# Performance work log

Measured on AMD Instinct MI355X. Metric: run time of the kernel, lower is better.

## Reference

```python
import jax, jax.numpy as jnp
import numpy as np

B, L, D, DF, E, R = 4, 1024, 1024, 4096, 32768, 64
EPS = 1e-6


def layer_norm(x, g, b, eps=EPS):
    mu = x.mean(-1, keepdims=True)
    var = ((x - mu) ** 2).mean(-1, keepdims=True)
    return (x - mu) * jax.lax.rsqrt(var + eps) * g + b


def setup_inputs() -> dict:
    key = jax.random.key(0)
    ks = jax.random.split(key, 16)
    s = 0.02
    return {
        "hidden_states": jax.random.normal(ks[0], (B, L, D), jnp.float32),
        "rel_table": jax.random.normal(ks[1], (R, D), jnp.float32) * s,
        "Wq": jax.random.normal(ks[2], (D, D), jnp.float32) * s,
        "bq": jnp.zeros((D,), jnp.float32),
        "Wk": jax.random.normal(ks[3], (D, D), jnp.float32) * s,
        "Wv": jax.random.normal(ks[4], (D, D), jnp.float32) * s,
        "Wo": jax.random.normal(ks[5], (D, D), jnp.float32) * s,
        "bo": jnp.zeros((D,), jnp.float32),
        "ln0_g": jnp.ones((D,), jnp.float32),
        "ln0_b": jnp.zeros((D,), jnp.float32),
        "ln1_g": jnp.ones((D,), jnp.float32),
        "ln1_b": jnp.zeros((D,), jnp.float32),
        "W1": jax.random.normal(ks[6], (D, DF), jnp.float32) * s,
        "b1": jnp.zeros((DF,), jnp.float32),
        "W2": jax.random.normal(ks[7], (DF, D), jnp.float32) * s,
        "b2": jnp.zeros((D,), jnp.float32),
        "ln2_g": jnp.ones((D,), jnp.float32),
        "ln2_b": jnp.zeros((D,), jnp.float32),
        "edge_src": jax.random.randint(ks[8], (B, E), 0, L, jnp.int32),
        "edge_dst": jax.random.randint(ks[9], (B, E), 0, L, jnp.int32),
        "edge_rel": jax.random.randint(ks[10], (B, E), 0, R, jnp.int32),
    }


def reference(hidden_states, rel_table, Wq, bq, Wk, Wv, Wo, bo,
              ln0_g, ln0_b, ln1_g, ln1_b, W1, b1, W2, b2, ln2_g, ln2_b,
              edge_src, edge_dst, edge_rel):
    scale = np.sqrt(D).astype(np.float32)  # num_heads=1 -> d_k = D
    hs_norm = layer_norm(hidden_states, ln0_g, ln0_b)

    def rgat_one(x, src, dst, rel):
        # x: [L, D]; src/dst/rel: [E]
        e = rel_table[rel]                       # [E, D] relation embeddings
        q = x @ Wq + bq
        k = x @ Wk
        v = x @ Wv
        score = jnp.sum((k[src] + e) * q[dst], axis=-1) / scale      # [E]
        score = jnp.exp(jnp.clip(score, -10.0, 10.0))
        wv = jax.ops.segment_sum((v[src] + e) * score[:, None], dst, num_segments=L)
        z = jax.ops.segment_sum(score, dst, num_segments=L)          # [L]
        o = wv / z[:, None]
        out = layer_norm(x + o @ Wo + bo, ln1_g, ln1_b)
        ffn = jnp.maximum(out @ W1 + b1, 0.0) @ W2 + b2
        return layer_norm(out + ffn, ln2_g, ln2_b)

    graph_rep = jax.vmap(rgat_one)(hs_norm, edge_src, edge_dst, edge_rel)
    out = jax.nn.elu(graph_rep)                  # dropout = identity (eval)
    return hidden_states + out
```

## Files before the change

### kernel.cpp

```cpp
#include <hip/hip_runtime.h>
#include <hip/hip_bf16.h>

#define B_SZ 4
#define L_SEQ 1024
#define D_MODEL 1024
#define DF_FF 4096
#define E_PER_B 32768
#define R_REL 64
#define M_ROWS (B_SZ * L_SEQ)

typedef __attribute__((ext_vector_type(8))) short bf16x8;
typedef __attribute__((ext_vector_type(4))) float f32x4;

__device__ inline float b2f(unsigned short u) {
    union { unsigned int i; float f; } x; x.i = ((unsigned int)u) << 16; return x.f;
}
__device__ inline unsigned short f2b(float f) {
    union { float f; unsigned int u; } x; x.f = f;
    unsigned int r = x.u + 0x7FFFu + ((x.u >> 16) & 1u);
    return (unsigned short)(r >> 16);
}

#define GLOBAL_CAST(p) ((const __attribute__((address_space(1))) void*)(p))
#define LDS_CAST(p)    ((__attribute__((address_space(3))) void*)(p))

__global__ void prep_all(const float* __restrict__ Wq, const float* __restrict__ Wk,
                         const float* __restrict__ Wv, const float* __restrict__ Wo,
                         const float* __restrict__ W1, const float* __restrict__ W2,
                         const float* __restrict__ rel, const float* __restrict__ bq,
                         unsigned short* __restrict__ Wqkv_t, unsigned short* __restrict__ Wo_t,
                         unsigned short* __restrict__ W1_t, unsigned short* __restrict__ W2_t,
                         unsigned short* __restrict__ relbPad, unsigned short* __restrict__ relbT,
                         float* __restrict__ bqkv) {
    __shared__ float tile[32][33];
    const int id = blockIdx.x, tid = threadIdx.x;
    if (id < 12288) {
        const float* src; unsigned short* dst; int K, N, x, y;
        if (id < 4096) {
            const int seg = id >> 10, t = id & 1023;
            K = 1024; N = 1024; x = t & 31; y = t >> 5;
            src = (seg == 0) ? Wq : (seg == 1) ? Wk : (seg == 2) ? Wv : Wo;
            dst = (seg == 3) ? Wo_t : (Wqkv_t + (size_t)seg * 1048576);
        } else if (id < 8192) {
            const int t = id - 4096; K = 1024; N = 4096; x = t & 127; y = t >> 7;
            src = W1; dst = W1_t;
        } else {
            const int t = id - 8192; K = 4096; N = 1024; x = t & 31; y = t >> 5;
            src = W2; dst = W2_t;
        }
        const int n0 = x * 32, k0 = y * 32, tx = tid & 31, ty = tid >> 5;
#pragma unroll
        for (int r = 0; r < 32; r += 8)
            tile[ty + r][tx] = src[(size_t)(k0 + ty + r) * N + (n0 + tx)];
        __syncthreads();
#pragma unroll
        for (int r = 0; r < 32; r += 8)
            dst[(size_t)(n0 + ty + r) * K + (k0 + tx)] = f2b(tile[tx][ty + r]);
    } else if (id < 12800) {
        const int i = (id - 12288) * 256 + tid;
        relbPad[i] = (i < 65536) ? f2b(rel[i]) : (unsigned short)0;
    } else if (id < 13056) {
        const int i = (id - 12800) * 256 + tid;
        relbT[i] = f2b(rel[(i & 63) * 1024 + (i >> 6)]);
    } else {
        const int i = (id - 13056) * 256 + tid;
        bqkv[i] = (i < 1024) ? bq[i] : 0.0f;
    }
}

__global__ void transpose_v_bf16(const unsigned short* __restrict__ QKV,
                                 unsigned short* __restrict__ Vt) {
    __shared__ unsigned short tile[32][33];
    const int b = blockIdx.z;
    const int d0 = blockIdx.x * 32, s0 = blockIdx.y * 32;
    const int tx = threadIdx.x & 31, ty = threadIdx.x >> 5;
#pragma unroll
    for (int r = 0; r < 32; r += 8)
        tile[ty + r][tx] = QKV[(size_t)((b << 10) + s0 + ty + r) * 3072 + 2048 + d0 + tx];
    __syncthreads();
#pragma unroll
    for (int r = 0; r < 32; r += 8)
        Vt[(size_t)b * 1048576 + (size_t)(d0 + ty + r) * 1024 + s0 + tx] = tile[tx][ty + r];
}

__device__ inline void tile_swizzle(int id, int ntn, int& tm, int& tn) {
    tm = ((id & 7) + ((id >> 3) / ntn) * 8) * 128;
    tn = ((id >> 3) % ntn) * 128;
}

template<bool OUT_BF16, bool RELU, bool ACC>
__global__ __launch_bounds__(256, 4)
void gemm_bf16(const unsigned short* __restrict__ A, int lda,
               const unsigned short* __restrict__ Bt, int ldb, size_t bt_batch,
               const float* __restrict__ bias,
               float* __restrict__ Cf, unsigned short* __restrict__ Cb,
               const float* __restrict__ accin,
               int N, int K, int ntn) {
    __shared__ unsigned short lA[128 * 64];
    __shared__ unsigned short lB[128 * 64];
    int tile_m, tile_n;
    tile_swizzle(blockIdx.x, ntn, tile_m, tile_n);
    const int t = threadIdx.x;
    const int wave = t >> 6, lane = t & 63;
    const int wm = (wave >> 1) * 64, wn = (wave & 1) * 64;
    const int quad = lane >> 4, l16 = lane & 15;

    const int srow = lane >> 3;
    const int schunk = ((lane & 7) ^ srow) * 8;
    const unsigned short* gA = A + (size_t)(tile_m + wave * 32 + srow) * lda + schunk;
    const unsigned short* gB = Bt + (size_t)(tile_m >> 10) * bt_batch
                                  + (size_t)(tile_n + wave * 32 + srow) * ldb + schunk;

    f32x4 acc[4][4];
#pragma unroll
    for (int i = 0; i < 4; i++)
#pragma unroll
        for (int j = 0; j < 4; j++) acc[i][j] = (f32x4)0.0f;

    for (int k0 = 0; k0 < K; k0 += 64) {
        __syncthreads();
#pragma unroll
        for (int r = 0; r < 4; ++r) {
            __builtin_amdgcn_global_load_lds(GLOBAL_CAST(gA + (size_t)r * 8 * lda),
                                             LDS_CAST(&lA[(wave * 32 + r * 8) * 64]), 16, 0, 0);
            __builtin_amdgcn_global_load_lds(GLOBAL_CAST(gB + (size_t)r * 8 * ldb),
                                             LDS_CAST(&lB[(wave * 32 + r * 8) * 64]), 16, 0, 0);
        }
        gA += 64; gB += 64;
        __builtin_amdgcn_s_waitcnt(0);
        __syncthreads();

#pragma unroll
        for (int kk = 0; kk < 2; ++kk) {
            const int cb = kk * 4 + quad;
            bf16x8 af[4], bf[4];
#pragma unroll
            for (int i = 0; i < 4; i++) {
                const int ra = wm + i * 16 + l16;
                af[i] = *(const bf16x8*)&lA[ra * 64 + ((cb ^ (ra & 7)) * 8)];
                const int rb = wn + i * 16 + l16;
                bf[i] = *(const bf16x8*)&lB[rb * 64 + ((cb ^ (rb & 7)) * 8)];
            }
#pragma unroll
            for (int mi = 0; mi < 4; mi++)
#pragma unroll
                for (int ni = 0; ni < 4; ni++)
                    acc[mi][ni] = __builtin_amdgcn_mfma_f32_16x16x32_bf16(af[mi], bf[ni], acc[mi][ni], 0, 0, 0);
        }
    }

#pragma unroll
    for (int mi = 0; mi < 4; mi++) {
#pragma unroll
        for (int ni = 0; ni < 4; ni++) {
            const int col = tile_n + wn + ni * 16 + l16;
            const float bv = bias[col];
#pragma unroll
            for (int r = 0; r < 4; r++) {
                const int row = tile_m + wm + mi * 16 + quad * 4 + r;
                float v = acc[mi][ni][r] + bv;
                if (ACC) v += accin[(size_t)row * N + col];
                if (RELU) v = fmaxf(v, 0.0f);
                if (OUT_BF16) Cb[(size_t)row * N + col] = f2b(v);
                else          Cf[(size_t)row * N + col] = v;
            }
        }
    }
}

__global__ __launch_bounds__(256, 4)
void gemm_bf16_splitk(const unsigned short* __restrict__ A, int lda,
                      const unsigned short* __restrict__ Bt, int ldb, size_t bt_batch,
                      const float* __restrict__ bias,
                      unsigned short* __restrict__ Pbase, size_t pstride,
                      int N, int Kc, int ntn) {
    __shared__ unsigned short lA[128 * 64];
    __shared__ unsigned short lB[128 * 64];
    int tile_m, tile_n;
    tile_swizzle(blockIdx.x, ntn, tile_m, tile_n);
    const int z = blockIdx.z;
    const int kofs = z * Kc;
    const int t = threadIdx.x;
    const int wave = t >> 6, lane = t & 63;
    const int wm = (wave >> 1) * 64, wn = (wave & 1) * 64;
    const int quad = lane >> 4, l16 = lane & 15;

    const int srow = lane >> 3;
    const int schunk = ((lane & 7) ^ srow) * 8;
    const unsigned short* gA = A + (size_t)(tile_m + wave * 32 + srow) * lda + kofs + schunk;
    const unsigned short* gB = Bt + (size_t)(tile_m >> 10) * bt_batch
                                  + (size_t)(tile_n + wave * 32 + srow) * ldb + kofs + schunk;

    f32x4 acc[4][4];
#pragma unroll
    for (int i = 0; i < 4; i++)
#pragma unroll
        for (int j = 0; j < 4; j++) acc[i][j] = (f32x4)0.0f;

    for (int k0 = 0; k0 < Kc; k0 += 64) {
        __syncthreads();
#pragma unroll
        for (int r = 0; r < 4; ++r) {
            __builtin_amdgcn_global_load_lds(GLOBAL_CAST(gA + (size_t)r * 8 * lda),
                                             LDS_CAST(&lA[(wave * 32 + r * 8) * 64]), 16, 0, 0);
            __builtin_amdgcn_global_load_lds(GLOBAL_CAST(gB + (size_t)r * 8 * ldb),
                                             LDS_CAST(&lB[(wave * 32 + r * 8) * 64]), 16, 0, 0);
        }
        gA += 64; gB += 64;
        __builtin_amdgcn_s_waitcnt(0);
        __syncthreads();

#pragma unroll
        for (int kk = 0; kk < 2; ++kk) {
            const int cb = kk * 4 + quad;
            bf16x8 af[4], bf[4];
#pragma unroll
            for (int i = 0; i < 4; i++) {
                const int ra = wm + i * 16 + l16;
                af[i] = *(const bf16x8*)&lA[ra * 64 + ((cb ^ (ra & 7)) * 8)];
                const int rb = wn + i * 16 + l16;
                bf[i] = *(const bf16x8*)&lB[rb * 64 + ((cb ^ (rb & 7)) * 8)];
            }
#pragma unroll
            for (int mi = 0; mi < 4; mi++)
#pragma unroll
                for (int ni = 0; ni < 4; ni++)
                    acc[mi][ni] = __builtin_amdgcn_mfma_f32_16x16x32_bf16(af[mi], bf[ni], acc[mi][ni], 0, 0, 0);
        }
    }

    unsigned short* P = Pbase + (size_t)z * pstride;
#pragma unroll
    for (int mi = 0; mi < 4; mi++) {
#pragma unroll
        for (int ni = 0; ni < 4; ni++) {
            const int col = tile_n + wn + ni * 16 + l16;
            const float bv = (z == 0) ? bias[col] : 0.0f;
#pragma unroll
            for (int r = 0; r < 4; r++) {
                const int row = tile_m + wm + mi * 16 + quad * 4 + r;
                P[(size_t)row * N + col] = f2b(acc[mi][ni][r] + bv);
            }
        }
    }
}

template<int MODE, int NR>
__global__ void ln_kernel(const float* __restrict__ X, const unsigned short* __restrict__ Xb,
                          const unsigned short* __restrict__ Rbase, size_t rstride,
                          const float* __restrict__ g, const float* __restrict__ be,
                          float* __restrict__ of32, unsigned short* __restrict__ ob16,
                          const float* __restrict__ hidden, float* __restrict__ fout) {
    __shared__ float sb1[4], sb2[4];
    const int row = blockIdx.x, t = threadIdx.x;
    const size_t base = (size_t)row * 1024 + t * 4;

    float x0, x1, x2, x3;
    if (MODE == 2) {
        ushort4 xv = *(const ushort4*)(Xb + base);
        x0 = b2f(xv.x); x1 = b2f(xv.y); x2 = b2f(xv.z); x3 = b2f(xv.w);
    } else {
        float4 xv = *(const float4*)(X + base);
        x0 = xv.x; x1 = xv.y; x2 = xv.z; x3 = xv.w;
    }
#pragma unroll
    for (int r = 0; r < NR; r++) {
        ushort4 rv = *(const ushort4*)(Rbase + r * rstride + base);
        x0 += b2f(rv.x); x1 += b2f(rv.y); x2 += b2f(rv.z); x3 += b2f(rv.w);
    }
    float s = x0 + x1 + x2 + x3;
#pragma unroll
    for (int o = 32; o > 0; o >>= 1) s += __shfl_down(s, o);
    if ((t & 63) == 0) sb1[t >> 6] = s;
    __syncthreads();
    const float mu = (sb1[0] + sb1[1] + sb1[2] + sb1[3]) * (1.0f / 1024.0f);

    const float d0 = x0 - mu, d1 = x1 - mu, d2 = x2 - mu, d3 = x3 - mu;
    float s2 = d0 * d0 + d1 * d1 + d2 * d2 + d3 * d3;
#pragma unroll
    for (int o = 32; o > 0; o >>= 1) s2 += __shfl_down(s2, o);
    if ((t & 63) == 0) sb2[t >> 6] = s2;
    __syncthreads();
    const float var = (sb2[0] + sb2[1] + sb2[2] + sb2[3]) * (1.0f / 1024.0f);
    const float rstd = rsqrtf(var + 1e-6f);

    const float4 gv = *(const float4*)(g + t * 4);
    const float4 bv = *(const float4*)(be + t * 4);
    const float y0 = d0 * rstd * gv.x + bv.x;
    const float y1 = d1 * rstd * gv.y + bv.y;
    const float y2 = d2 * rstd * gv.z + bv.z;
    const float y3 = d3 * rstd * gv.w + bv.w;

    if (MODE == 0) {
        float4 o; o.x = y0; o.y = y1; o.z = y2; o.w = y3;
        *(float4*)(of32 + base) = o;
    }
    if (MODE <= 1) {
        ushort4 ob; ob.x = f2b(y0); ob.y = f2b(y1); ob.z = f2b(y2); ob.w = f2b(y3);
        *(ushort4*)(ob16 + base) = ob;
    } else {
        const float4 hv = *(const float4*)(hidden + base);
        const float e0 = y0 > 0.0f ? y0 : expm1f(y0);
        const float e1 = y1 > 0.0f ? y1 : expm1f(y1);
        const float e2 = y2 > 0.0f ? y2 : expm1f(y2);
        const float e3 = y3 > 0.0f ? y3 : expm1f(y3);
        float4 o; o.x = hv.x + e0; o.y = hv.y + e1; o.z = hv.z + e2; o.w = hv.w + e3;
        *(float4*)(fout + base) = o;
    }
}

__global__ void edge_scatter(const unsigned short* __restrict__ S0h,
                             const unsigned short* __restrict__ S1h,
                             const float* __restrict__ T,
                             const int* __restrict__ src, const int* __restrict__ dst,
                             const int* __restrict__ rel,
                             float* __restrict__ A, float* __restrict__ G) {
    const int gg = blockIdx.x * 256 + threadIdx.x;
    const int b = gg >> 15;
    const int s = src[gg], d = dst[gg], r = rel[gg];
    const size_t srow = (size_t)((b << 10) + s) * 1024 + d;
    const float sval = b2f(S0h[srow]) + b2f(S1h[srow]);
    const float tval = T[(size_t)((b << 10) + d) * 128 + r];
    float sc = (sval + tval) * (1.0f / 32.0f);
    sc = expf(fminf(fmaxf(sc, -10.0f), 10.0f));
    atomicAdd(&A[((size_t)((b << 10) + d) << 10) + s], sc);
    atomicAdd(&G[((size_t)((b << 10) + d) << 6) + r], sc);
}

__global__ void normalize(const float* __restrict__ A, const float* __restrict__ G,
                          unsigned short* __restrict__ An, unsigned short* __restrict__ Gn) {
    __shared__ float sInv;
    const int row = blockIdx.x, t = threadIdx.x;
    float v = 0.0f;
    if (t < 64) {
        v = G[(size_t)row * 64 + t];
        float s = v;
#pragma unroll
        for (int o = 1; o < 64; o <<= 1) s += __shfl_xor(s, o);
        if (t == 0) sInv = 1.0f / s;
    }
    __syncthreads();
    const float inv = sInv;
    if (t < 64) Gn[(size_t)row * 64 + t] = f2b(v * inv);
    const size_t base = (size_t)row * 1024 + t * 4;
    const float4 a = *(const float4*)(A + base);
    ushort4 o;
    o.x = f2b(a.x * inv); o.y = f2b(a.y * inv); o.z = f2b(a.z * inv); o.w = f2b(a.w * inv);
    *(ushort4*)(An + base) = o;
}

extern "C" void kernel_launch(void* const* d_in, const int* in_sizes, int n_in,
                              void* d_out, int out_size, void* d_ws, size_t ws_size,
                              hipStream_t stream) {
    const float* hidden  = (const float*)d_in[0];
    const float* rel_tbl = (const float*)d_in[1];
    const float* Wq = (const float*)d_in[2];
    const float* bq = (const float*)d_in[3];
    const float* Wk = (const float*)d_in[4];
    const float* Wv = (const float*)d_in[5];
    const float* Wo = (const float*)d_in[6];
    const float* bo = (const float*)d_in[7];
    const float* ln0_g = (const float*)d_in[8];
    const float* ln0_b = (const float*)d_in[9];
    const float* ln1_g = (const float*)d_in[10];
    const float* ln1_b = (const float*)d_in[11];
    const float* W1 = (const float*)d_in[12];
    const float* b1 = (const float*)d_in[13];
    const float* W2 = (const float*)d_in[14];
    const float* b2 = (const float*)d_in[15];
    const float* ln2_g = (const float*)d_in[16];
    const float* ln2_b = (const float*)d_in[17];
    const int* esrc = (const int*)d_in[18];
    const int* edst = (const int*)d_in[19];
    const int* erel = (const int*)d_in[20];
    float* out = (float*)d_out;

    char* ws = (char*)d_ws;
    const size_t MB = 1024 * 1024;
    float*          Xn_f32  = (float*)(ws + 0);
    unsigned short* Xn_b16  = (unsigned short*)(ws + 16 * MB);
    unsigned short* Vt      = (unsigned short*)(ws + 16 * MB);
    unsigned short* H1      = (unsigned short*)(ws + 0);
    unsigned short* Wqkv_t  = (unsigned short*)(ws + 24 * MB);
    unsigned short* Wo_t    = (unsigned short*)(ws + 30 * MB);
    unsigned short* W1_t    = (unsigned short*)(ws + 32 * MB);
    unsigned short* W2_t    = (unsigned short*)(ws + 40 * MB);
    unsigned short* relbPad = (unsigned short*)(ws + 48 * MB);
    unsigned short* relbT   = (unsigned short*)(ws + 48 * MB + 256 * 1024);
    float*          bqkv    = (float*)(ws + 48 * MB + 512 * 1024);
    const float*    zbias   = bqkv + 1024;
    unsigned short* QKV     = (unsigned short*)(ws + 49 * MB);
    float*          Amat    = (float*)(ws + 49 * MB);
    float*          Gmat    = (float*)(ws + 65 * MB);
    unsigned short* PwoH    = (unsigned short*)(ws + 49 * MB);
    unsigned short* Qw2H    = (unsigned short*)(ws + 49 * MB);
    unsigned short* S0h     = (unsigned short*)(ws + 73 * MB);
    float*          tmp     = (float*)(ws + 73 * MB);
    unsigned short* Obf     = (unsigned short*)(ws + 89 * MB);
    unsigned short* An      = (unsigned short*)(ws + 97 * MB);
    float*          Tmat    = (float*)(ws + 105 * MB);
    unsigned short* Gn      = (unsigned short*)(ws + 105 * MB);
    unsigned short* Out_b16 = (unsigned short*)(ws + 113 * MB);

    const size_t PSTRIDE_H = 4u * 1024 * 1024;
    const size_t BT_QKV  = 1024u * 3072;
    const size_t BT_VT   = 1024u * 1024;
    const dim3 blk(256);

    prep_all<<<13068, blk, 0, stream>>>(Wq, Wk, Wv, Wo, W1, W2, rel_tbl, bq,
                                        Wqkv_t, Wo_t, W1_t, W2_t, relbPad, relbT, bqkv);
    ln_kernel<0, 0><<<M_ROWS, blk, 0, stream>>>(hidden, nullptr, nullptr, 0, ln0_g, ln0_b,
                                                Xn_f32, Xn_b16, nullptr, nullptr);
    gemm_bf16<true, false, false><<<dim3(24 * 32), blk, 0, stream>>>(
        Xn_b16, 1024, Wqkv_t, 1024, 0, bqkv, nullptr, QKV, nullptr, 3072, 1024, 24);
    transpose_v_bf16<<<dim3(32, 32, 4), blk, 0, stream>>>(QKV, Vt);
    gemm_bf16_splitk<<<dim3(8 * 32, 1, 2), blk, 0, stream>>>(
        QKV + 1024, 3072, QKV, 3072, BT_QKV, zbias, S0h, PSTRIDE_H, 1024, 512, 8);
    gemm_bf16<false, false, false><<<dim3(1 * 32), blk, 0, stream>>>(
        QKV, 3072, relbPad, 1024, 0, zbias, Tmat, nullptr, nullptr, 128, 1024, 1);
    hipMemsetAsync(ws + 49 * MB, 0, 17 * MB, stream);
    edge_scatter<<<512, blk, 0, stream>>>(S0h, S0h + PSTRIDE_H, Tmat, esrc, edst, erel, Amat, Gmat);
    normalize<<<M_ROWS, blk, 0, stream>>>(Amat, Gmat, An, Gn);
    gemm_bf16<false, false, false><<<dim3(8 * 32), blk, 0, stream>>>(
        Gn, 64, relbT, 64, 0, zbias, tmp, nullptr, nullptr, 1024, 64, 8);
    gemm_bf16<true, false, true><<<dim3(8 * 32), blk, 0, stream>>>(
        An, 1024, Vt, 1024, BT_VT, zbias, nullptr, Obf, tmp, 1024, 1024, 8);
    gemm_bf16_splitk<<<dim3(8 * 32, 1, 2), blk, 0, stream>>>(
        Obf, 1024, Wo_t, 1024, 0, bo, PwoH, PSTRIDE_H, 1024, 512, 8);
    ln_kernel<1, 2><<<M_ROWS, blk, 0, stream>>>(Xn_f32, nullptr, PwoH, PSTRIDE_H, ln1_g, ln1_b,
                                                nullptr, Out_b16, nullptr, nullptr);
    gemm_bf16<true, true, false><<<dim3(32 * 32), blk, 0, stream>>>(
        Out_b16, 1024, W1_t, 1024, 0, b1, nullptr, H1, nullptr, 4096, 1024, 32);
    gemm_bf16_splitk<<<dim3(8 * 32, 1, 4), blk, 0, stream>>>(
        H1, 4096, W2_t, 4096, 0, b2, Qw2H, PSTRIDE_H, 1024, 1024, 8);
    ln_kernel<2, 4><<<M_ROWS, blk, 0, stream>>>(nullptr, Out_b16, Qw2H, PSTRIDE_H, ln2_g, ln2_b,
                                                nullptr, nullptr, hidden, out);
    (void)in_sizes; (void)n_in; (void)out_size; (void)ws_size;
}
```

Before: 402.0 us.

## Fuse relation-term GEMMs into extended score and aggregation GEMMs

The K·Q score GEMM and the Q·rel table GEMM are merged into one extended GEMM (1152 rows per batch) whose output layout lets the edge scatter read both terms from one buffer. The aggregation now concatenates the attention matrix with the normalized relation weights along K (1088 wide) and the transposed V with the transposed relation table, so a single GEMM replaces the small G·rel GEMM plus the accumulate-in pass. This removes two launches and an fp32 intermediate round trip. In exchange the relation term is now stored in bf16 instead of fp32, and K=1088 is not a multiple of 128, which relies on the GEMM handling a 64-step K.

```diff
diff --git a/kernel.cpp b/kernel.cpp
--- a/kernel.cpp
+++ b/kernel.cpp
@@ -24,13 +24,18 @@
 #define GLOBAL_CAST(p) ((const __attribute__((address_space(1))) void*)(p))
 #define LDS_CAST(p)    ((__attribute__((address_space(3))) void*)(p))
 
+#define LDB_WV 1088
+#define BT_WV  (1024u * 1088u)
+#define BT_QKV (1024u * 3072u)
+#define SEXT_M 1152
+
 __global__ void prep_all(const float* __restrict__ Wq, const float* __restrict__ Wk,
                          const float* __restrict__ Wv, const float* __restrict__ Wo,
                          const float* __restrict__ W1, const float* __restrict__ W2,
                          const float* __restrict__ rel, const float* __restrict__ bq,
                          unsigned short* __restrict__ Wqkv_t, unsigned short* __restrict__ Wo_t,
                          unsigned short* __restrict__ W1_t, unsigned short* __restrict__ W2_t,
-                         unsigned short* __restrict__ relbPad, unsigned short* __restrict__ relbT,
+                         unsigned short* __restrict__ relbPad, unsigned short* __restrict__ Bwv,
                          float* __restrict__ bqkv) {
     __shared__ float tile[32][33];
     const int id = blockIdx.x, tid = threadIdx.x;
@@ -59,17 +64,18 @@
     } else if (id < 12800) {
         const int i = (id - 12288) * 256 + tid;
         relbPad[i] = (i < 65536) ? f2b(rel[i]) : (unsigned short)0;
-    } else if (id < 13056) {
+    } else if (id < 13824) {
         const int i = (id - 12800) * 256 + tid;
-        relbT[i] = f2b(rel[(i & 63) * 1024 + (i >> 6)]);
+        const int b = i >> 16, rem = i & 65535, d = rem >> 6, r = rem & 63;
+        Bwv[(size_t)b * BT_WV + (size_t)d * LDB_WV + 1024 + r] = f2b(rel[r * 1024 + d]);
     } else {
-        const int i = (id - 13056) * 256 + tid;
+        const int i = (id - 13824) * 256 + tid;
         bqkv[i] = (i < 1024) ? bq[i] : 0.0f;
     }
 }
 
 __global__ void transpose_v_bf16(const unsigned short* __restrict__ QKV,
-                                 unsigned short* __restrict__ Vt) {
+                                 unsigned short* __restrict__ Bwv) {
     __shared__ unsigned short tile[32][33];
     const int b = blockIdx.z;
     const int d0 = blockIdx.x * 32, s0 = blockIdx.y * 32;
@@ -80,7 +86,7 @@
     __syncthreads();
 #pragma unroll
     for (int r = 0; r < 32; r += 8)
-        Vt[(size_t)b * 1048576 + (size_t)(d0 + ty + r) * 1024 + s0 + tx] = tile[tx][ty + r];
+        Bwv[(size_t)b * BT_WV + (size_t)(d0 + ty + r) * LDB_WV + s0 + tx] = tile[tx][ty + r];
 }
 
 __device__ inline void tile_swizzle(int id, int ntn, int& tm, int& tn) {
@@ -88,13 +94,12 @@
     tn = ((id >> 3) % ntn) * 128;
 }
 
-template<bool OUT_BF16, bool RELU, bool ACC>
+template<bool OUT_BF16, bool RELU>
 __global__ __launch_bounds__(256, 4)
 void gemm_bf16(const unsigned short* __restrict__ A, int lda,
                const unsigned short* __restrict__ Bt, int ldb, size_t bt_batch,
                const float* __restrict__ bias,
                float* __restrict__ Cf, unsigned short* __restrict__ Cb,
-               const float* __restrict__ accin,
                int N, int K, int ntn) {
     __shared__ unsigned short lA[128 * 64];
     __shared__ unsigned short lB[128 * 64];
@@ -159,7 +164,6 @@
             for (int r = 0; r < 4; r++) {
                 const int row = tile_m + wm + mi * 16 + quad * 4 + r;
                 float v = acc[mi][ni][r] + bv;
-                if (ACC) v += accin[(size_t)row * N + col];
                 if (RELU) v = fmaxf(v, 0.0f);
                 if (OUT_BF16) Cb[(size_t)row * N + col] = f2b(v);
                 else          Cf[(size_t)row * N + col] = v;
@@ -245,6 +249,89 @@
     }
 }
 
+__global__ __launch_bounds__(256, 4)
+void gemm_sext(const unsigned short* __restrict__ QKV,
+               const unsigned short* __restrict__ relPad,
+               unsigned short* __restrict__ Pbase, int Kc) {
+    __shared__ unsigned short lA[128 * 64];
+    __shared__ unsigned short lB[128 * 64];
+    const int bx = blockIdx.x, b = blockIdx.y, z = blockIdx.z;
+    const int tile_m = (bx >> 3) * 128;
+    const int tile_n = (bx & 7) * 128;
+    const int kofs = z * Kc;
+    const int t = threadIdx.x;
+    const int wave = t >> 6, lane = t & 63;
+    const int wm = (wave >> 1) * 64, wn = (wave & 1) * 64;
+    const int quad = lane >> 4, l16 = lane & 15;
+
+    const int srow = lane >> 3;
+    const int schunk = ((lane & 7) ^ srow) * 8;
+    const int arow = tile_m + wave * 32 + srow;
+    const unsigned short* gA;
+    size_t lda;
+    if (tile_m < 1024) {
+        gA = QKV + (size_t)b * BT_QKV + (size_t)arow * 3072 + 1024 + kofs + schunk;
+        lda = 3072;
+    } else {
+        gA = relPad + (size_t)(arow - 1024) * 1024 + kofs + schunk;
+        lda = 1024;
+    }
+    const unsigned short* gB = QKV + (size_t)b * BT_QKV
+                                   + (size_t)(tile_n + wave * 32 + srow) * 3072 + kofs + schunk;
+
+    f32x4 acc[4][4];
+#pragma unroll
+    for (int i = 0; i < 4; i++)
+#pragma unroll
+        for (int j = 0; j < 4; j++) acc[i][j] = (f32x4)0.0f;
+
+    for (int k0 = 0; k0 < Kc; k0 += 64) {
+        __syncthreads();
+#pragma unroll
+        for (int r = 0; r < 4; ++r) {
+            __builtin_amdgcn_global_load_lds(GLOBAL_CAST(gA + (size_t)r * 8 * lda),
+                                             LDS_CAST(&lA[(wave * 32 + r * 8) * 64]), 16, 0, 0);
+            __builtin_amdgcn_global_load_lds(GLOBAL_CAST(gB + (size_t)r * 8 * 3072),
+                                             LDS_CAST(&lB[(wave * 32 + r * 8) * 64]), 16, 0, 0);
+        }
+        gA += 64; gB += 64;
+        __builtin_amdgcn_s_waitcnt(0);
+        __syncthreads();
+
+#pragma unroll
+        for (int kk = 0; kk < 2; ++kk) {
+            const int cb = kk * 4 + quad;
+            bf16x8 af[4], bf[4];
+#pragma unroll
+            for (int i = 0; i < 4; i++) {
+                const int ra = wm + i * 16 + l16;
+                af[i] = *(const bf16x8*)&lA[ra * 64 + ((cb ^ (ra & 7)) * 8)];
+                const int rb = wn + i * 16 + l16;
+                bf[i] = *(const bf16x8*)&lB[rb * 64 + ((cb ^ (rb & 7)) * 8)];
+            }
+#pragma unroll
+            for (int mi = 0; mi < 4; mi++)
+#pragma unroll
+                for (int ni = 0; ni < 4; ni++)
+                    acc[mi][ni] = __builtin_amdgcn_mfma_f32_16x16x32_bf16(af[mi], bf[ni], acc[mi][ni], 0, 0, 0);
+        }
+    }
+
+    unsigned short* P = Pbase + ((size_t)z * B_SZ + b) * (SEXT_M * 1024);
+#pragma unroll
+    for (int mi = 0; mi < 4; mi++) {
+#pragma unroll
+        for (int ni = 0; ni < 4; ni++) {
+            const int col = tile_n + wn + ni * 16 + l16;
+#pragma unroll
+            for (int r = 0; r < 4; r++) {
+                const int row = tile_m + wm + mi * 16 + quad * 4 + r;
+                P[(size_t)row * 1024 + col] = f2b(acc[mi][ni][r]);
+            }
+        }
+    }
+}
+
 template<int MODE, int NR>
 __global__ void ln_kernel(const float* __restrict__ X, const unsigned short* __restrict__ Xb,
                           const unsigned short* __restrict__ Rbase, size_t rstride,
@@ -309,18 +396,18 @@
     }
 }
 
-__global__ void edge_scatter(const unsigned short* __restrict__ S0h,
-                             const unsigned short* __restrict__ S1h,
-                             const float* __restrict__ T,
+__global__ void edge_scatter(const unsigned short* __restrict__ S,
                              const int* __restrict__ src, const int* __restrict__ dst,
                              const int* __restrict__ rel,
                              float* __restrict__ A, float* __restrict__ G) {
+    const size_t ZSTR = (size_t)B_SZ * SEXT_M * 1024;
     const int gg = blockIdx.x * 256 + threadIdx.x;
     const int b = gg >> 15;
     const int s = src[gg], d = dst[gg], r = rel[gg];
-    const size_t srow = (size_t)((b << 10) + s) * 1024 + d;
-    const float sval = b2f(S0h[srow]) + b2f(S1h[srow]);
-    const float tval = T[(size_t)((b << 10) + d) * 128 + r];
+    const size_t sbase = ((size_t)b * SEXT_M + s) * 1024 + d;
+    const size_t tbase = ((size_t)b * SEXT_M + 1024 + r) * 1024 + d;
+    const float sval = b2f(S[sbase]) + b2f(S[sbase + ZSTR]);
+    const float tval = b2f(S[tbase]) + b2f(S[tbase + ZSTR]);
     float sc = (sval + tval) * (1.0f / 32.0f);
     sc = expf(fminf(fmaxf(sc, -10.0f), 10.0f));
     atomicAdd(&A[((size_t)((b << 10) + d) << 10) + s], sc);
@@ -328,7 +415,7 @@
 }
 
 __global__ void normalize(const float* __restrict__ A, const float* __restrict__ G,
-                          unsigned short* __restrict__ An, unsigned short* __restrict__ Gn) {
+                          unsigned short* __restrict__ Awv) {
     __shared__ float sInv;
     const int row = blockIdx.x, t = threadIdx.x;
     float v = 0.0f;
@@ -341,12 +428,18 @@
     }
     __syncthreads();
     const float inv = sInv;
-    if (t < 64) Gn[(size_t)row * 64 + t] = f2b(v * inv);
-    const size_t base = (size_t)row * 1024 + t * 4;
-    const float4 a = *(const float4*)(A + base);
+    const size_t obase = (size_t)row * LDB_WV;
+    const float4 a = *(const float4*)(A + (size_t)row * 1024 + t * 4);
     ushort4 o;
     o.x = f2b(a.x * inv); o.y = f2b(a.y * inv); o.z = f2b(a.z * inv); o.w = f2b(a.w * inv);
-    *(ushort4*)(An + base) = o;
+    *(ushort4*)(Awv + obase + t * 4) = o;
+    if (t < 16) {
+        const float4 gq = *(const float4*)(G + (size_t)row * 64 + t * 4);
+        ushort4 og;
+        og.x = f2b(gq.x * inv); og.y = f2b(gq.y * inv);
+        og.z = f2b(gq.z * inv); og.w = f2b(gq.w * inv);
+        *(ushort4*)(Awv + obase + 1024 + t * 4) = og;
+    }
 }
 
 extern "C" void kernel_launch(void* const* d_in, const int* in_sizes, int n_in,
@@ -379,58 +472,47 @@
     const size_t MB = 1024 * 1024;
     float*          Xn_f32  = (float*)(ws + 0);
     unsigned short* Xn_b16  = (unsigned short*)(ws + 16 * MB);
-    unsigned short* Vt      = (unsigned short*)(ws + 16 * MB);
     unsigned short* H1      = (unsigned short*)(ws + 0);
     unsigned short* Wqkv_t  = (unsigned short*)(ws + 24 * MB);
     unsigned short* Wo_t    = (unsigned short*)(ws + 30 * MB);
     unsigned short* W1_t    = (unsigned short*)(ws + 32 * MB);
     unsigned short* W2_t    = (unsigned short*)(ws + 40 * MB);
     unsigned short* relbPad = (unsigned short*)(ws + 48 * MB);
-    unsigned short* relbT   = (unsigned short*)(ws + 48 * MB + 256 * 1024);
     float*          bqkv    = (float*)(ws + 48 * MB + 512 * 1024);
     const float*    zbias   = bqkv + 1024;
     unsigned short* QKV     = (unsigned short*)(ws + 49 * MB);
-    float*          Amat    = (float*)(ws + 49 * MB);
-    float*          Gmat    = (float*)(ws + 65 * MB);
-    unsigned short* PwoH    = (unsigned short*)(ws + 49 * MB);
+    unsigned short* Awv     = (unsigned short*)(ws + 49 * MB);
+    unsigned short* Obf     = (unsigned short*)(ws + 58 * MB);
     unsigned short* Qw2H    = (unsigned short*)(ws + 49 * MB);
-    unsigned short* S0h     = (unsigned short*)(ws + 73 * MB);
-    float*          tmp     = (float*)(ws + 73 * MB);
-    unsigned short* Obf     = (unsigned short*)(ws + 89 * MB);
-    unsigned short* An      = (unsigned short*)(ws + 97 * MB);
-    float*          Tmat    = (float*)(ws + 105 * MB);
-    unsigned short* Gn      = (unsigned short*)(ws + 105 * MB);
+    unsigned short* PwoH    = (unsigned short*)(ws + 66 * MB);
+    unsigned short* SxH     = (unsigned short*)(ws + 73 * MB);
+    unsigned short* Bwv     = (unsigned short*)(ws + 92 * MB);
+    float*          Amat    = (float*)(ws + 101 * MB);
+    float*          Gmat    = (float*)(ws + 117 * MB);
     unsigned short* Out_b16 = (unsigned short*)(ws + 113 * MB);
 
     const size_t PSTRIDE_H = 4u * 1024 * 1024;
-    const size_t BT_QKV  = 1024u * 3072;
-    const size_t BT_VT   = 1024u * 1024;
     const dim3 blk(256);
 
-    prep_all<<<13068, blk, 0, stream>>>(Wq, Wk, Wv, Wo, W1, W2, rel_tbl, bq,
-                                        Wqkv_t, Wo_t, W1_t, W2_t, relbPad, relbT, bqkv);
+    prep_all<<<13836, blk, 0, stream>>>(Wq, Wk, Wv, Wo, W1, W2, rel_tbl, bq,
+                                        Wqkv_t, Wo_t, W1_t, W2_t, relbPad, Bwv, bqkv);
     ln_kernel<0, 0><<<M_ROWS, blk, 0, stream>>>(hidden, nullptr, nullptr, 0, ln0_g, ln0_b,
                                                 Xn_f32, Xn_b16, nullptr, nullptr);
-    gemm_bf16<true, false, false><<<dim3(24 * 32), blk, 0, stream>>>(
-        Xn_b16, 1024, Wqkv_t, 1024, 0, bqkv, nullptr, QKV, nullptr, 3072, 1024, 24);
-    transpose_v_bf16<<<dim3(32, 32, 4), blk, 0, stream>>>(QKV, Vt);
-    gemm_bf16_splitk<<<dim3(8 * 32, 1, 2), blk, 0, stream>>>(
-        QKV + 1024, 3072, QKV, 3072, BT_QKV, zbias, S0h, PSTRIDE_H, 1024, 512, 8);
-    gemm_bf16<false, false, false><<<dim3(1 * 32), blk, 0, stream>>>(
-        QKV, 3072, relbPad, 1024, 0, zbias, Tmat, nullptr, nullptr, 128, 1024, 1);
-    hipMemsetAsync(ws + 49 * MB, 0, 17 * MB, stream);
-    edge_scatter<<<512, blk, 0, stream>>>(S0h, S0h + PSTRIDE_H, Tmat, esrc, edst, erel, Amat, Gmat);
-    normalize<<<M_ROWS, blk, 0, stream>>>(Amat, Gmat, An, Gn);
-    gemm_bf16<false, false, false><<<dim3(8 * 32), blk, 0, stream>>>(
-        Gn, 64, relbT, 64, 0, zbias, tmp, nullptr, nullptr, 1024, 64, 8);
-    gemm_bf16<true, false, true><<<dim3(8 * 32), blk, 0, stream>>>(
-        An, 1024, Vt, 1024, BT_VT, zbias, nullptr, Obf, tmp, 1024, 1024, 8);
+    gemm_bf16<true, false><<<dim3(24 * 32), blk, 0, stream>>>(
+        Xn_b16, 1024, Wqkv_t, 1024, 0, bqkv, nullptr, QKV, 3072, 1024, 24);
+    transpose_v_bf16<<<dim3(32, 32, 4), blk, 0, stream>>>(QKV, Bwv);
+    gemm_sext<<<dim3(72, B_SZ, 2), blk, 0, stream>>>(QKV, relbPad, SxH, 512);
+    hipMemsetAsync(ws + 101 * MB, 0, 17 * MB, stream);
+    edge_scatter<<<512, blk, 0, stream>>>(SxH, esrc, edst, erel, Amat, Gmat);
+    normalize<<<M_ROWS, blk, 0, stream>>>(Amat, Gmat, Awv);
+    gemm_bf16<true, false><<<dim3(8 * 32), blk, 0, stream>>>(
+        Awv, LDB_WV, Bwv, LDB_WV, BT_WV, zbias, nullptr, Obf, 1024, LDB_WV, 8);
     gemm_bf16_splitk<<<dim3(8 * 32, 1, 2), blk, 0, stream>>>(
         Obf, 1024, Wo_t, 1024, 0, bo, PwoH, PSTRIDE_H, 1024, 512, 8);
     ln_kernel<1, 2><<<M_ROWS, blk, 0, stream>>>(Xn_f32, nullptr, PwoH, PSTRIDE_H, ln1_g, ln1_b,
                                                 nullptr, Out_b16, nullptr, nullptr);
-    gemm_bf16<true, true, false><<<dim3(32 * 32), blk, 0, stream>>>(
-        Out_b16, 1024, W1_t, 1024, 0, b1, nullptr, H1, nullptr, 4096, 1024, 32);
+    gemm_bf16<true, true><<<dim3(32 * 32), blk, 0, stream>>>(
+        Out_b16, 1024, W1_t, 1024, 0, b1, nullptr, H1, 4096, 1024, 32);
     gemm_bf16_splitk<<<dim3(8 * 32, 1, 4), blk, 0, stream>>>(
         H1, 4096, W2_t, 4096, 0, b2, Qw2H, PSTRIDE_H, 1024, 1024, 8);
     ln_kernel<2, 4><<<M_ROWS, blk, 0, stream>>>(nullptr, Out_b16, Qw2H, PSTRIDE_H, ln2_g, ln2_b,
```

Result: faster. 376.5 us (-6.3%).
